# Optimization experiments

Measured on AMD Instinct MI355X. Metric: run time of the kernel, lower is better.

The kernel has to match this reference:

```python
import math
import jax, jax.numpy as jnp
import numpy as np

B, N, D_FULL, M, D_V = 8, 4096, 256, 256, 256


def _phi(x, omega):
    # x: [..., N, d_full], omega: [M, d_full] -> [..., N, M]
    proj = x @ omega.T
    log_phi = proj - 0.5 * jnp.sum(x * x, axis=-1, keepdims=True)
    log_phi = log_phi - jnp.max(log_phi, axis=-1, keepdims=True)
    return jnp.exp(log_phi) / math.sqrt(omega.shape[0])


def _causal(phi_q, phi_k, V):
    # phi_q/phi_k: [B, N, M], V: [B, N, d_v]
    b, n, m = phi_q.shape
    d_v = V.shape[-1]

    def step(carry, inp):
        S, z = carry
        pq, pk, v = inp  # [B,M], [B,M], [B,d_v]
        S = S + pk[:, :, None] * v[:, None, :]          # [B, M, d_v]
        z = z + pk                                       # [B, M]
        num = jnp.einsum('bi,bij->bj', pq, S)            # [B, d_v]
        den = jnp.maximum(jnp.sum(pq * z, axis=-1), 1e-6)
        return (S, z), num / den[:, None]

    S0 = jnp.zeros((b, m, d_v), phi_q.dtype)
    z0 = jnp.zeros((b, m), phi_q.dtype)
    xs = (jnp.swapaxes(phi_q, 0, 1), jnp.swapaxes(phi_k, 0, 1), jnp.swapaxes(V, 0, 1))
    _, ys = jax.lax.scan(step, (S0, z0), xs)  # ys: [N, B, d_v]
    return jnp.swapaxes(ys, 0, 1)


def setup_inputs() -> dict:
    key = jax.random.key(0)
    kq, kk, kv, ko = jax.random.split(key, 4)
    Q = jax.random.normal(kq, (B, N, D_FULL), dtype=jnp.float32)
    K_in = jax.random.normal(kk, (B, N, D_FULL), dtype=jnp.float32)
    V = jax.random.normal(kv, (B, N, D_V), dtype=jnp.float32)
    omega = jax.random.normal(ko, (M, D_FULL), dtype=jnp.float32)
    return {"Q": Q, "K_in": K_in, "V": V, "omega": omega, "causal": 1}


def reference(Q, K_in, V, omega, causal):
    phi_q = _phi(Q, omega)
    phi_k = _phi(K_in, omega)
    if causal:
        return _causal(phi_q, phi_k, V)
    S = jnp.einsum('bni,bnj->bij', phi_k, V)          # [B, M, d_v]
    z = jnp.sum(phi_k, axis=-2)                        # [B, M]
    num = jnp.einsum('bni,bij->bnj', phi_q, S)
    den = jnp.maximum(jnp.einsum('bni,bi->bn', phi_q, z), 1e-6)
    return num / den[..., None]
```

## Files before the change

kernel.cpp:

```cpp
#include <hip/hip_runtime.h>

#define BN 8
#define NN 4096
#define DD 256
#define MM 256
#define DV 256
#define CHUNK 256
#define NC (NN / CHUNK)

using f32x4 = __attribute__((ext_vector_type(4))) float;
using s16x8 = __attribute__((ext_vector_type(8))) short;

#define MFMA16(a, b, c) __builtin_amdgcn_mfma_f32_16x16x32_bf16(a, b, c, 0, 0, 0)

__device__ __forceinline__ unsigned short f2bf(float x) {
    union { float f; unsigned int u; } v; v.f = x;
    unsigned int r = v.u + 0x7FFF + ((v.u >> 16) & 1);
    return (unsigned short)(r >> 16);
}
__device__ __forceinline__ float bf2f(unsigned short u) {
    union { unsigned int u; float f; } v; v.u = ((unsigned int)u) << 16;
    return v.f;
}

__device__ __forceinline__ void split8(const float4 xa, const float4 xb,
                                       s16x8& ah, s16x8& al)
{
    const float xs[8] = {xa.x, xa.y, xa.z, xa.w, xb.x, xb.y, xb.z, xb.w};
#pragma unroll
    for (int j = 0; j < 8; ++j) {
        union { float f; unsigned u; } v; v.f = xs[j];
        const unsigned hm = v.u & 0xFFFF0000u;
        union { unsigned u; float f; } hv; hv.u = hm;
        ah[j] = (short)(hm >> 16);
        al[j] = (short)f2bf(xs[j] - hv.f);
    }
}

__global__ __launch_bounds__(256) void omconv(
    const float* __restrict__ Om, unsigned short* __restrict__ OmH,
    unsigned short* __restrict__ OmL)
{
    const int i = blockIdx.x * 256 + threadIdx.x;
    const float4 v = *(const float4*)(Om + (size_t)i * 4);
    const float xs[4] = {v.x, v.y, v.z, v.w};
    unsigned short h[4], l[4];
#pragma unroll
    for (int j = 0; j < 4; ++j) {
        h[j] = f2bf(xs[j]);
        l[j] = f2bf(xs[j] - bf2f(h[j]));
    }
    *(uint2*)(OmH + (size_t)i * 4) = *(uint2*)h;
    *(uint2*)(OmL + (size_t)i * 4) = *(uint2*)l;
}

__global__ __launch_bounds__(256) void phi_fused(
    const float* __restrict__ Qp, const float* __restrict__ Kp,
    const unsigned short* __restrict__ OmH, const unsigned short* __restrict__ OmL,
    unsigned short* __restrict__ PhiQ, unsigned short* __restrict__ PhiK,
    unsigned short* __restrict__ PhiT, float* __restrict__ Zp)
{
    const int tid = threadIdx.x;
    const int w = tid >> 6;
    const int lane = tid & 63;
    const int col = lane & 15, quad = lane >> 4;
    const bool kpath = blockIdx.x < 512;
    const int id = kpath ? blockIdx.x : (blockIdx.x - 512);
    const float* __restrict__ X = kpath ? Kp : Qp;
    unsigned short* __restrict__ Phi = kpath ? PhiK : PhiQ;
    const long r0 = (long)id * 64;

    __shared__ __align__(16) char lds[66560];
    __shared__ float rowmax_s[64];
    float (*Xs)[260] = (float(*)[260])lds;
    unsigned short (*P)[264] = (unsigned short(*)[264])lds;
    unsigned int* P32 = (unsigned int*)lds;
    float (*red)[67] = (float(*)[67])(lds + 34048);

    {
        const float* gbase = X + r0 * DD + (size_t)lane * 4;
#pragma unroll
        for (int j = 0; j < 16; ++j) {
            const int row = w * 16 + j;
            __builtin_amdgcn_global_load_lds(
                (const __attribute__((address_space(1))) unsigned int*)(gbase + (size_t)row * DD),
                (__attribute__((address_space(3))) unsigned int*)(&Xs[row][0]),
                16, 0, 0);
        }
    }
    __syncthreads();

    f32x4 acc[4][4] = {};
    s16x8 bh0[4], bl0[4], bh1[4], bl1[4];
#pragma unroll
    for (int ct = 0; ct < 4; ++ct) {
        const size_t off = (size_t)(w * 64 + ct * 16 + col) * DD + quad * 8;
        bh0[ct] = *(const s16x8*)(OmH + off);
        bl0[ct] = *(const s16x8*)(OmL + off);
    }
#pragma unroll
    for (int kt = 0; kt < 8; ++kt) {
        if (kt < 7) {
#pragma unroll
            for (int ct = 0; ct < 4; ++ct) {
                const size_t off = (size_t)(w * 64 + ct * 16 + col) * DD + (kt + 1) * 32 + quad * 8;
                bh1[ct] = *(const s16x8*)(OmH + off);
                bl1[ct] = *(const s16x8*)(OmL + off);
            }
        }
#pragma unroll
        for (int t = 0; t < 4; ++t) {
            const float4 xa = *(const float4*)&Xs[t * 16 + col][kt * 32 + quad * 8];
            const float4 xb = *(const float4*)&Xs[t * 16 + col][kt * 32 + quad * 8 + 4];
            s16x8 ah, al;
            split8(xa, xb, ah, al);
#pragma unroll
            for (int ct = 0; ct < 4; ++ct) {
                acc[t][ct] = MFMA16(ah, bh0[ct], acc[t][ct]);
                acc[t][ct] = MFMA16(ah, bl0[ct], acc[t][ct]);
                acc[t][ct] = MFMA16(al, bh0[ct], acc[t][ct]);
            }
        }
#pragma unroll
        for (int ct = 0; ct < 4; ++ct) { bh0[ct] = bh1[ct]; bl0[ct] = bl1[ct]; }
    }

    __syncthreads();
#pragma unroll
    for (int t = 0; t < 4; ++t)
#pragma unroll
        for (int r = 0; r < 4; ++r) {
            float m = acc[t][0][r];
#pragma unroll
            for (int ct = 1; ct < 4; ++ct) m = fmaxf(m, acc[t][ct][r]);
            red[t * 16 + quad * 4 + r][w * 16 + col] = m;
        }
    __syncthreads();
    if (tid < 64) {
        float m = red[tid][0];
#pragma unroll
        for (int j = 1; j < 64; ++j) m = fmaxf(m, red[tid][j]);
        rowmax_s[tid] = m;
    }
    __syncthreads();

#pragma unroll
    for (int t = 0; t < 4; ++t)
#pragma unroll
        for (int r = 0; r < 4; ++r) {
            const int n = t * 16 + quad * 4 + r;
            const float rm = rowmax_s[n];
#pragma unroll
            for (int ct = 0; ct < 4; ++ct) {
                const float val = __expf(acc[t][ct][r] - rm) * 0.0625f;
                const unsigned u = (unsigned)f2bf(val);
                const unsigned up = (unsigned)__shfl_xor((int)u, 1);
                if ((col & 1) == 0)
                    P32[n * 132 + w * 32 + ct * 8 + (col >> 1)] = u | (up << 16);
            }
        }
    __syncthreads();

    {
        const int t7 = tid & 7;
        const int nb = tid >> 3;
#pragma unroll
        for (int p2 = 0; p2 < 2; ++p2) {
            const int n = p2 * 32 + nb;
#pragma unroll
            for (int s = 0; s < 4; ++s)
                *(uint4*)(Phi + (r0 + n) * MM + t7 * 8 + s * 64) =
                    *(const uint4*)&P[n][t7 * 8 + s * 64];
        }
    }

    if (kpath) {
        const int b = id >> 6;
        const int c = (id >> 2) & 15;
        const int n0 = (int)(r0 & (NN - 1));
        const int m0 = tid & 31;
        const int nsub = tid >> 5;
#pragma unroll
        for (int mi = 0; mi < 8; ++mi) {
            const int m = mi * 32 + m0;
            unsigned short u[8];
#pragma unroll
            for (int j = 0; j < 8; ++j) u[j] = P[nsub * 8 + j][m];
            *(uint4*)(PhiT + ((size_t)b * MM + m) * NN + n0 + nsub * 8) = *(uint4*)u;
        }
        float z = 0.f;
#pragma unroll
        for (int n = 0; n < 64; ++n) z += bf2f(P[n][tid]);
        atomicAdd(&Zp[((b * NC + c) << 8) + tid], z);
    }
}

__global__ __launch_bounds__(256) void transpose_v(
    const float* __restrict__ V, unsigned short* __restrict__ VT)
{
    const int tid = threadIdx.x;
    const int ct = blockIdx.x & 3;
    const long r0 = (long)(blockIdx.x >> 2) * 64;
    const int b = (int)(r0 >> 12);
    const int n0 = (int)(r0 & (NN - 1));
    __shared__ unsigned short T[64][72];
    const int rr = tid >> 4, cs = tid & 15;
#pragma unroll
    for (int p = 0; p < 4; ++p) {
        const int r = p * 16 + rr;
        const float4 v = *(const float4*)(V + (r0 + r) * DV + ct * 64 + cs * 4);
        T[cs * 4 + 0][r] = f2bf(v.x); T[cs * 4 + 1][r] = f2bf(v.y);
        T[cs * 4 + 2][r] = f2bf(v.z); T[cs * 4 + 3][r] = f2bf(v.w);
    }
    __syncthreads();
    const int cl = tid >> 3, ns = tid & 7;
#pragma unroll
    for (int p = 0; p < 2; ++p) {
        const int c = p * 32 + cl;
        *(uint4*)(VT + ((size_t)b * DV + ct * 64 + c) * NN + n0 + ns * 8) = *(uint4*)&T[c][ns * 8];
    }
}

__global__ __launch_bounds__(256, 3) void state_mfma(
    const unsigned short* __restrict__ VT, const unsigned short* __restrict__ PkT,
    unsigned short* __restrict__ ST)
{
    const int tid = threadIdx.x;
    const int w = tid >> 6;
    const int lane = tid & 63;
    const int col = lane & 15, quad = lane >> 4;
    const int q  = blockIdx.x >> 7;
    const int bc = blockIdx.x & 127;
    const int c  = bc & 15;
    const int b  = bc >> 4;
    const int dv0 = (q & 1) * 128 + (w & 1) * 64;
    const int m0  = (q >> 1) * 128 + (w >> 1) * 64;
    const unsigned short* Ab = VT  + (size_t)b * DV * NN + (size_t)c * CHUNK;
    const unsigned short* Bb = PkT + (size_t)b * MM * NN + (size_t)c * CHUNK;

    f32x4 acc[4][4] = {};
    s16x8 a0[4], b0[4], a1[4], b1[4];
#pragma unroll
    for (int t = 0; t < 4; ++t) {
        a0[t] = *(const s16x8*)(Ab + (size_t)(dv0 + t * 16 + col) * NN + quad * 8);
        b0[t] = *(const s16x8*)(Bb + (size_t)(m0 + t * 16 + col) * NN + quad * 8);
    }
#pragma unroll
    for (int kt = 0; kt < 8; ++kt) {
        if (kt < 7) {
#pragma unroll
            for (int t = 0; t < 4; ++t) {
                a1[t] = *(const s16x8*)(Ab + (size_t)(dv0 + t * 16 + col) * NN + (kt + 1) * 32 + quad * 8);
                b1[t] = *(const s16x8*)(Bb + (size_t)(m0 + t * 16 + col) * NN + (kt + 1) * 32 + quad * 8);
            }
        }
#pragma unroll
        for (int i = 0; i < 4; ++i)
#pragma unroll
            for (int j = 0; j < 4; ++j) acc[i][j] = MFMA16(a0[i], b0[j], acc[i][j]);
#pragma unroll
        for (int t = 0; t < 4; ++t) { a0[t] = a1[t]; b0[t] = b1[t]; }
    }
    unsigned short* Sb = ST + (((size_t)(b * NC + c)) << 16);
#pragma unroll
    for (int i = 0; i < 4; ++i)
#pragma unroll
        for (int j = 0; j < 4; ++j)
#pragma unroll
            for (int r = 0; r < 4; ++r)
                Sb[(dv0 + i * 16 + quad * 4 + r) * MM + m0 + j * 16 + col] = f2bf(acc[i][j][r]);
}

__global__ __launch_bounds__(256) void prefix2(
    unsigned short* __restrict__ ST, float* __restrict__ Z)
{
    const long idx = (long)blockIdx.x * 256 + threadIdx.x;
    const int b = (int)(idx >> 16);
    const int r = (int)(idx & 65535);
    float run = 0.f;
#pragma unroll
    for (int c = 0; c < NC; ++c) {
        const size_t off = (((size_t)(b * NC + c)) << 16) + r;
        const float v = bf2f(ST[off]);
        ST[off] = f2bf(run);
        run += v;
    }
    if (idx < BN * MM) {
        const int b2 = (int)(idx >> 8);
        const int m = (int)(idx & 255);
        float rz = 0.f;
#pragma unroll
        for (int c = 0; c < NC; ++c) {
            const size_t off = (size_t)(b2 * NC + c) * MM + m;
            const float v = Z[off];
            Z[off] = rz;
            rz += v;
        }
    }
}

__global__ __launch_bounds__(256) void out_mfma(
    const unsigned short* __restrict__ PhiQ, const unsigned short* __restrict__ PhiK,
    const unsigned short* __restrict__ VT, const unsigned short* __restrict__ ST,
    const float* __restrict__ Z, float* __restrict__ Out)
{
    const int tid = threadIdx.x;
    const int w = tid >> 6;
    const int lane = tid & 63;
    const int col = lane & 15, quad = lane >> 4;
    const int it = 3 - (blockIdx.x >> 7);
    const int low = blockIdx.x & 127;
    const int c  = low & 15;
    const int b  = low >> 4;
    const size_t chunk_row = (size_t)b * NN + (size_t)c * CHUNK;
    const unsigned short* Qrow = PhiQ + (chunk_row + it * 64) * MM;

    __shared__ unsigned short Qs[64][264];
    __shared__ unsigned short A_s[64][72];
    __shared__ float red[64][68];
    __shared__ float z_s[256];
    __shared__ float den_s[64];

    const float zval = Z[((size_t)(b * NC + c) << 8) + tid];
    s16x8 bk0[8], bk1[8];
#pragma unroll
    for (int ms = 0; ms < 8; ++ms)
        bk0[ms] = *(const s16x8*)(PhiK + (chunk_row)*MM + (size_t)(w * 16 + col) * MM + ms * 32 + quad * 8);
    uint4 qv[8];
#pragma unroll
    for (int i = 0; i < 8; ++i)
        qv[i] = *((const uint4*)Qrow + i * 256 + tid);
    z_s[tid] = zval;
#pragma unroll
    for (int i = 0; i < 8; ++i) {
        const int f = i * 256 + tid;
        *(uint4*)&Qs[f >> 5][(f & 31) * 8] = qv[i];
    }
    __syncthreads();

    f32x4 oacc[4][4] = {};
    float rsum[4][4] = {};

    for (int jt = 0; jt <= it; ++jt) {
        s16x8 bv[8];
        const unsigned short* Vbase = VT + ((size_t)b * DV + w * 64) * NN + (size_t)c * CHUNK + jt * 64;
#pragma unroll
        for (int ks2 = 0; ks2 < 2; ++ks2)
#pragma unroll
            for (int t2 = 0; t2 < 4; ++t2)
                bv[ks2 * 4 + t2] = *(const s16x8*)(Vbase + (size_t)(t2 * 16 + col) * NN + ks2 * 32 + quad * 8);
        f32x4 accA[4] = {};
#pragma unroll
        for (int ms = 0; ms < 8; ++ms)
#pragma unroll
            for (int t = 0; t < 4; ++t) {
                const s16x8 aq = *(const s16x8*)&Qs[t * 16 + col][ms * 32 + quad * 8];
                accA[t] = MFMA16(aq, bk0[ms], accA[t]);
            }
        if (jt < it) {
            const unsigned short* Krn = PhiK + (chunk_row + (jt + 1) * 64) * MM;
#pragma unroll
            for (int ms = 0; ms < 8; ++ms)
                bk1[ms] = *(const s16x8*)(Krn + (size_t)(w * 16 + col) * MM + ms * 32 + quad * 8);
        }
        __syncthreads();
#pragma unroll
        for (int t = 0; t < 4; ++t)
#pragma unroll
            for (int r = 0; r < 4; ++r) {
                const int i_loc = t * 16 + quad * 4 + r;
                const int j_loc = w * 16 + col;
                float v = (jt * 64 + j_loc <= it * 64 + i_loc) ? accA[t][r] : 0.f;
                rsum[t][r] += v;
                A_s[i_loc][j_loc] = f2bf(v);
            }
        __syncthreads();
#pragma unroll
        for (int ks2 = 0; ks2 < 2; ++ks2) {
            s16x8 av[4];
#pragma unroll
            for (int t = 0; t < 4; ++t)
                av[t] = *(const s16x8*)&A_s[t * 16 + col][ks2 * 32 + quad * 8];
#pragma unroll
            for (int t2 = 0; t2 < 4; ++t2)
#pragma unroll
                for (int t = 0; t < 4; ++t)
                    oacc[t][t2] = MFMA16(av[t], bv[ks2 * 4 + t2], oacc[t][t2]);
        }
#pragma unroll
        for (int ms = 0; ms < 8; ++ms) bk0[ms] = bk1[ms];
    }
#pragma unroll
    for (int t = 0; t < 4; ++t)
#pragma unroll
        for (int r = 0; r < 4; ++r)
            red[t * 16 + quad * 4 + r][w * 16 + col] = rsum[t][r];

    const unsigned short* Sb = ST + (((size_t)(b * NC + c)) << 16) + (size_t)(w * 64) * MM;
    s16x8 bs0[4], bs1[4];
#pragma unroll
    for (int t2 = 0; t2 < 4; ++t2)
        bs0[t2] = *(const s16x8*)(Sb + (size_t)(t2 * 16 + col) * MM + quad * 8);
#pragma unroll
    for (int ms = 0; ms < 8; ++ms) {
        if (ms < 7) {
#pragma unroll
            for (int t2 = 0; t2 < 4; ++t2)
                bs1[t2] = *(const s16x8*)(Sb + (size_t)(t2 * 16 + col) * MM + (ms + 1) * 32 + quad * 8);
        }
        s16x8 aq[4];
#pragma unroll
        for (int t = 0; t < 4; ++t)
            aq[t] = *(const s16x8*)&Qs[t * 16 + col][ms * 32 + quad * 8];
#pragma unroll
        for (int t2 = 0; t2 < 4; ++t2)
#pragma unroll
            for (int t = 0; t < 4; ++t)
                oacc[t][t2] = MFMA16(aq[t], bs0[t2], oacc[t][t2]);
#pragma unroll
        for (int t2 = 0; t2 < 4; ++t2) bs0[t2] = bs1[t2];
    }
    {
        const int i = tid & 63;
        const int seg = tid >> 6;
        float d = 0.f;
#pragma unroll
        for (int g = 0; g < 8; ++g) {
            const s16x8 qv8 = *(const s16x8*)&Qs[i][seg * 64 + g * 8];
#pragma unroll
            for (int x = 0; x < 8; ++x)
                d = fmaf(bf2f((unsigned short)qv8[x]), z_s[seg * 64 + g * 8 + x], d);
        }
        red[i][64 + seg] = d;
    }
    __syncthreads();
    if (tid < 64) {
        float s = 0.f;
#pragma unroll
        for (int j = 0; j < 68; ++j) s += red[tid][j];
        den_s[tid] = fmaxf(s, 1e-6f);
    }
    __syncthreads();
#pragma unroll
    for (int t = 0; t < 4; ++t)
#pragma unroll
        for (int r = 0; r < 4; ++r) {
            const int i_loc = t * 16 + quad * 4 + r;
            const float invd = 1.0f / den_s[i_loc];
#pragma unroll
            for (int t2 = 0; t2 < 4; ++t2)
                Out[(chunk_row + it * 64 + i_loc) * DV + w * 64 + t2 * 16 + col] = oacc[t][t2][r] * invd;
        }
}

extern "C" void kernel_launch(void* const* d_in, const int* in_sizes, int n_in,
                              void* d_out, int out_size, void* d_ws, size_t ws_size,
                              hipStream_t stream)
{
    const float* Q  = (const float*)d_in[0];
    const float* K  = (const float*)d_in[1];
    const float* V  = (const float*)d_in[2];
    const float* Om = (const float*)d_in[3];
    float* out = (float*)d_out;

    const size_t NM = (size_t)BN * NN * MM;
    unsigned short* PhiQ  = (unsigned short*)d_ws;
    unsigned short* PhiK  = PhiQ + NM;
    unsigned short* PhiKT = PhiK + NM;
    unsigned short* VT    = PhiKT + NM;
    unsigned short* ST    = VT + NM;
    unsigned short* OmH   = ST + (size_t)BN * NC * DV * MM;
    unsigned short* OmL   = OmH + (size_t)MM * DD;
    float* Z = (float*)(OmL + (size_t)MM * DD);

    hipMemsetAsync(Z, 0, (size_t)BN * NC * MM * sizeof(float), stream);
    omconv<<<dim3(64), dim3(256), 0, stream>>>(Om, OmH, OmL);
    phi_fused<<<dim3(1024), dim3(256), 0, stream>>>(Q, K, OmH, OmL, PhiQ, PhiK, PhiKT, Z);
    transpose_v<<<dim3((BN * NN) / 64 * 4), dim3(256), 0, stream>>>(V, VT);
    state_mfma<<<dim3(BN * NC * 4), dim3(256), 0, stream>>>(VT, PhiKT, ST);
    prefix2<<<dim3((BN * DV * MM) / 256), dim3(256), 0, stream>>>(ST, Z);
    out_mfma<<<dim3(BN * NC * 4), dim3(256), 0, stream>>>(PhiQ, PhiK, VT, ST, Z, out);
}
```

Baseline: 246.8 us.

## Halve phi tile to 32 rows, pre-split bf16 into LDS, raise occupancy

```diff
diff --git a/kernel.cpp b/kernel.cpp
--- a/kernel.cpp
+++ b/kernel.cpp
@@ -54,7 +54,7 @@
     *(uint2*)(OmL + (size_t)i * 4) = *(uint2*)l;
 }
 
-__global__ __launch_bounds__(256) void phi_fused(
+__global__ __launch_bounds__(256, 4) void phi_fused(
     const float* __restrict__ Qp, const float* __restrict__ Kp,
     const unsigned short* __restrict__ OmH, const unsigned short* __restrict__ OmL,
     unsigned short* __restrict__ PhiQ, unsigned short* __restrict__ PhiK,
@@ -64,33 +64,41 @@
     const int w = tid >> 6;
     const int lane = tid & 63;
     const int col = lane & 15, quad = lane >> 4;
-    const bool kpath = blockIdx.x < 512;
-    const int id = kpath ? blockIdx.x : (blockIdx.x - 512);
+    const bool kpath = blockIdx.x < 1024;
+    const int id = kpath ? blockIdx.x : (blockIdx.x - 1024);
     const float* __restrict__ X = kpath ? Kp : Qp;
     unsigned short* __restrict__ Phi = kpath ? PhiK : PhiQ;
-    const long r0 = (long)id * 64;
-
-    __shared__ __align__(16) char lds[66560];
-    __shared__ float rowmax_s[64];
-    float (*Xs)[260] = (float(*)[260])lds;
-    unsigned short (*P)[264] = (unsigned short(*)[264])lds;
-    unsigned int* P32 = (unsigned int*)lds;
-    float (*red)[67] = (float(*)[67])(lds + 34048);
+    const long r0 = (long)id * 32;
+
+    __shared__ __align__(16) short AhS[32][264];
+    __shared__ __align__(16) short AlS[32][264];
+    __shared__ float rowmax_s[32];
+    float (*red)[68] = (float(*)[68])AhS;
+    unsigned short (*P)[264] = (unsigned short(*)[264])AlS;
+    unsigned int* P32 = (unsigned int*)AlS;
 
     {
-        const float* gbase = X + r0 * DD + (size_t)lane * 4;
-#pragma unroll
-        for (int j = 0; j < 16; ++j) {
-            const int row = w * 16 + j;
-            __builtin_amdgcn_global_load_lds(
-                (const __attribute__((address_space(1))) unsigned int*)(gbase + (size_t)row * DD),
-                (__attribute__((address_space(3))) unsigned int*)(&Xs[row][0]),
-                16, 0, 0);
-        }
-    }
-    __syncthreads();
-
-    f32x4 acc[4][4] = {};
+        const int rsub = lane >> 5;
+        const int cc = lane & 31;
+        float4 va[4], vb[4];
+#pragma unroll
+        for (int j = 0; j < 4; ++j) {
+            const int row = w * 8 + j * 2 + rsub;
+            const float* p = X + (r0 + row) * DD + cc * 8;
+            va[j] = *(const float4*)p;
+            vb[j] = *(const float4*)(p + 4);
+        }
+#pragma unroll
+        for (int j = 0; j < 4; ++j) {
+            const int row = w * 8 + j * 2 + rsub;
+            s16x8 ah, al;
+            split8(va[j], vb[j], ah, al);
+            *(s16x8*)&AhS[row][cc * 8] = ah;
+            *(s16x8*)&AlS[row][cc * 8] = al;
+        }
+    }
+
+    f32x4 acc[2][4] = {};
     s16x8 bh0[4], bl0[4], bh1[4], bl1[4];
 #pragma unroll
     for (int ct = 0; ct < 4; ++ct) {
@@ -98,6 +106,8 @@
         bh0[ct] = *(const s16x8*)(OmH + off);
         bl0[ct] = *(const s16x8*)(OmL + off);
     }
+    __syncthreads();
+
 #pragma unroll
     for (int kt = 0; kt < 8; ++kt) {
         if (kt < 7) {
@@ -109,11 +119,9 @@
             }
         }
 #pragma unroll
-        for (int t = 0; t < 4; ++t) {
-            const float4 xa = *(const float4*)&Xs[t * 16 + col][kt * 32 + quad * 8];
-            const float4 xb = *(const float4*)&Xs[t * 16 + col][kt * 32 + quad * 8 + 4];
-            s16x8 ah, al;
-            split8(xa, xb, ah, al);
+        for (int t = 0; t < 2; ++t) {
+            const s16x8 ah = *(const s16x8*)&AhS[t * 16 + col][kt * 32 + quad * 8];
+            const s16x8 al = *(const s16x8*)&AlS[t * 16 + col][kt * 32 + quad * 8];
 #pragma unroll
             for (int ct = 0; ct < 4; ++ct) {
                 acc[t][ct] = MFMA16(ah, bh0[ct], acc[t][ct]);
@@ -127,7 +135,7 @@
 
     __syncthreads();
 #pragma unroll
-    for (int t = 0; t < 4; ++t)
+    for (int t = 0; t < 2; ++t)
 #pragma unroll
         for (int r = 0; r < 4; ++r) {
             float m = acc[t][0][r];
@@ -136,16 +144,20 @@
             red[t * 16 + quad * 4 + r][w * 16 + col] = m;
         }
     __syncthreads();
-    if (tid < 64) {
-        float m = red[tid][0];
-#pragma unroll
-        for (int j = 1; j < 64; ++j) m = fmaxf(m, red[tid][j]);
-        rowmax_s[tid] = m;
-    }
-    __syncthreads();
-
-#pragma unroll
-    for (int t = 0; t < 4; ++t)
+    {
+        const int row = tid >> 3, seg = tid & 7;
+        float m = red[row][seg * 8];
+#pragma unroll
+        for (int j = 1; j < 8; ++j) m = fmaxf(m, red[row][seg * 8 + j]);
+        m = fmaxf(m, __shfl_xor(m, 1));
+        m = fmaxf(m, __shfl_xor(m, 2));
+        m = fmaxf(m, __shfl_xor(m, 4));
+        if (seg == 0) rowmax_s[row] = m;
+    }
+    __syncthreads();
+
+#pragma unroll
+    for (int t = 0; t < 2; ++t)
 #pragma unroll
         for (int r = 0; r < 4; ++r) {
             const int n = t * 16 + quad * 4 + r;
@@ -165,32 +177,28 @@
         const int t7 = tid & 7;
         const int nb = tid >> 3;
 #pragma unroll
-        for (int p2 = 0; p2 < 2; ++p2) {
-            const int n = p2 * 32 + nb;
-#pragma unroll
-            for (int s = 0; s < 4; ++s)
-                *(uint4*)(Phi + (r0 + n) * MM + t7 * 8 + s * 64) =
-                    *(const uint4*)&P[n][t7 * 8 + s * 64];
-        }
+        for (int s = 0; s < 4; ++s)
+            *(uint4*)(Phi + (r0 + nb) * MM + t7 * 8 + s * 64) =
+                *(const uint4*)&P[nb][t7 * 8 + s * 64];
     }
 
     if (kpath) {
-        const int b = id >> 6;
-        const int c = (id >> 2) & 15;
-        const int n0 = (int)(r0 & (NN - 1));
+        const int b = id >> 7;
+        const int c = (id >> 3) & 15;
+        const int n0 = (id & 127) * 32;
         const int m0 = tid & 31;
         const int nsub = tid >> 5;
 #pragma unroll
         for (int mi = 0; mi < 8; ++mi) {
             const int m = mi * 32 + m0;
-            unsigned short u[8];
-#pragma unroll
-            for (int j = 0; j < 8; ++j) u[j] = P[nsub * 8 + j][m];
-            *(uint4*)(PhiT + ((size_t)b * MM + m) * NN + n0 + nsub * 8) = *(uint4*)u;
+            unsigned short u[4];
+#pragma unroll
+            for (int j = 0; j < 4; ++j) u[j] = P[nsub * 4 + j][m];
+            *(uint2*)(PhiT + ((size_t)b * MM + m) * NN + n0 + nsub * 4) = *(uint2*)u;
         }
         float z = 0.f;
 #pragma unroll
-        for (int n = 0; n < 64; ++n) z += bf2f(P[n][tid]);
+        for (int n = 0; n < 32; ++n) z += bf2f(P[n][tid]);
         atomicAdd(&Zp[((b * NC + c) << 8) + tid], z);
     }
 }
@@ -475,7 +483,7 @@
 
     hipMemsetAsync(Z, 0, (size_t)BN * NC * MM * sizeof(float), stream);
     omconv<<<dim3(64), dim3(256), 0, stream>>>(Om, OmH, OmL);
-    phi_fused<<<dim3(1024), dim3(256), 0, stream>>>(Q, K, OmH, OmL, PhiQ, PhiK, PhiKT, Z);
+    phi_fused<<<dim3(2048), dim3(256), 0, stream>>>(Q, K, OmH, OmL, PhiQ, PhiK, PhiKT, Z);
     transpose_v<<<dim3((BN * NN) / 64 * 4), dim3(256), 0, stream>>>(V, VT);
     state_mfma<<<dim3(BN * NC * 4), dim3(256), 0, stream>>>(VT, PhiKT, ST);
     prefix2<<<dim3((BN * DV * MM) / 256), dim3(256), 0, stream>>>(ST, Z);
```

Result: slower. 266.8 us (+8.1%).
